# Kernel tuning notes

Hardware: AMD Instinct MI355X
Metric: run time of the kernel (lower is better)

The kernel has to match this reference:

```python
import jax, jax.numpy as jnp
import numpy as np

N = 524288          # total nodes (64 graphs x 8192 nodes)
E = 8388608         # total edges (avg degree 16)
F = 128             # num_features
H = 8               # hidden_size
B = 64              # num_graphs
NPG = N // B        # nodes per graph


def setup_inputs() -> dict:
    key = jax.random.key(0)
    ks = jax.random.split(key, 14)
    def lin(k, fan_in, shape):
        return (jax.random.normal(k, shape, jnp.float32) / np.float32(np.sqrt(fan_in)))
    return {
        "x": jax.random.normal(ks[0], (N, F), jnp.float32),
        "edge_index": jax.random.randint(ks[1], (2, E), 0, N, jnp.int32),
        "target_id": jax.random.randint(ks[2], (B,), 0, NPG, jnp.int32),
        "W1": lin(ks[3], F, (F, H)), "b1": jnp.zeros((H,), jnp.float32),
        "W2": lin(ks[4], H, (H, H)), "b2": jnp.zeros((H,), jnp.float32),
        "W3": lin(ks[5], H, (H, 1)), "b3": jnp.zeros((1,), jnp.float32),
        "Wl1": lin(ks[6], 2 * H + 1, (2 * H + 1, 16)), "bl1": jnp.zeros((16,), jnp.float32),
        "Wl2": lin(ks[7], 16, (16, 2)), "bl2": jnp.zeros((2,), jnp.float32),
    }


def reference(x, edge_index, target_id, W1, b1, W2, b2, W3, b3, Wl1, bl1, Wl2, bl2):
    src, dst = edge_index[0], edge_index[1]
    # GCN symmetric normalization with self-loops: deg includes the self-loop.
    deg = jax.ops.segment_sum(jnp.ones((E,), x.dtype), dst, num_segments=N) + 1.0
    dis = jax.lax.rsqrt(deg)                       # deg^{-1/2}, [N]
    norm = dis[src] * dis[dst]                     # per-edge coefficient, [E]

    def gcn_conv(h, W, b):
        h = h @ W                                  # [N, out]
        agg = jax.ops.segment_sum(h[src] * norm[:, None], dst, num_segments=N)
        # self-loop contribution has coefficient dis[i]*dis[i] = 1/deg[i]
        return agg + h * (dis * dis)[:, None] + b

    x1 = jax.nn.relu(gcn_conv(x, W1, b1))          # [N, 8]
    x2 = jax.nn.relu(gcn_conv(x1, W2, b2))         # [N, 8]
    x3 = jax.nn.relu(gcn_conv(x2, W3, b3))         # [N, 1]
    feats = jnp.concatenate([x1, x2, x3], axis=1)  # [N, 17]

    # per-graph target node: global index = graph_offset + local target_id
    idx = jnp.arange(B, dtype=jnp.int32) * NPG + target_id   # [B]
    z = jax.nn.relu(feats[idx] @ Wl1 + bl1)        # [B, 16]
    return z @ Wl2 + bl2                           # [B, 2]
```

## Files before the change

kernel.cpp:

```cpp
#include <hip/hip_runtime.h>
#include <cstdint>

#define N_NODES 524288
#define E_EDGES 8388608
#define F_IN 128
#define HID 8
#define B_GRAPHS 64
#define NPG 8192
#define NPG_SHIFT 13

#define BUCKETS 256
#define BSHIFT 11
#define BNODES 2048
#define BMASK 2047
#define SBLK 512
#define STHREADS 512
#define EPB (E_EDGES / SBLK)
#define CAP 160
#define EB_STRIDE (SBLK * CAP)
#define CSR_CAP 36864

__global__ void clear_kernel(int4* __restrict__ p) {
    p[blockIdx.x * blockDim.x + threadIdx.x] = make_int4(0, 0, 0, 0);
}

__global__ __launch_bounds__(STHREADS) void scatter_kernel(
        const int* __restrict__ src, const int* __restrict__ dst,
        unsigned int* __restrict__ ebuf, int* __restrict__ sc) {
    __shared__ int cur[BUCKETS];
    int t = threadIdx.x;
    if (t < BUCKETS) cur[t] = 0;
    __syncthreads();
    int eb = blockIdx.x * EPB;
    size_t blkoff = (size_t)blockIdx.x * CAP;
    #pragma unroll 4
    for (int k = 0; k < EPB / STHREADS; ++k) {
        int e = eb + k * STHREADS + t;
        int d = dst[e];
        int s = src[e];
        int b = d >> BSHIFT;
        int p = atomicAdd(&cur[b], 1);
        if (p < CAP)
            ebuf[(size_t)b * EB_STRIDE + blkoff + p] =
                ((unsigned int)(d & BMASK) << 19) | (unsigned int)s;
    }
    __syncthreads();
    if (t < BUCKETS) sc[t * SBLK + blockIdx.x] = (cur[t] < CAP) ? cur[t] : CAP;
}

__global__ __launch_bounds__(256) void build_kernel(const unsigned int* __restrict__ ebuf,
                                                    const int* __restrict__ sc,
                                                    int2* __restrict__ rowptr,
                                                    float* __restrict__ dis,
                                                    int* __restrict__ csr) {
    __shared__ int scs[SBLK];
    __shared__ int cnt[BNODES];
    __shared__ int cur[BNODES];
    __shared__ int tsum[256];
    int t = threadIdx.x;
    int b = blockIdx.x;
    for (int j = t; j < SBLK; j += 256) scs[j] = sc[b * SBLK + j];
    for (int j = t; j < BNODES; j += 256) cnt[j] = 0;
    __syncthreads();
    const unsigned int* eb = ebuf + (size_t)b * EB_STRIDE;
    int wv = t >> 6, ln = t & 63;
    for (int ss = wv; ss < SBLK; ss += 4) {
        int n = scs[ss];
        const unsigned int* p = eb + ss * CAP;
        for (int k = ln; k < n; k += 64)
            atomicAdd(&cnt[p[k] >> 19], 1);
    }
    __syncthreads();
    int v[8], loc[8], s = 0;
    #pragma unroll
    for (int k2 = 0; k2 < 8; ++k2) { v[k2] = cnt[t * 8 + k2]; loc[k2] = s; s += v[k2]; }
    tsum[t] = s;
    __syncthreads();
    for (int o = 1; o < 256; o <<= 1) {
        int y = (t >= o) ? tsum[t - o] : 0;
        __syncthreads();
        tsum[t] += y;
        __syncthreads();
    }
    int off = (t == 0) ? 0 : tsum[t - 1];
    int cbase = b * CSR_CAP;
    #pragma unroll
    for (int k2 = 0; k2 < 8; ++k2) {
        int j = t * 8 + k2;
        int st = off + loc[k2];
        cur[j] = st;
        rowptr[b * BNODES + j] = make_int2(cbase + st, cbase + st + v[k2]);
        dis[b * BNODES + j] = rsqrtf((float)v[k2] + 1.0f);
    }
    __syncthreads();
    for (int ss = wv; ss < SBLK; ss += 4) {
        int n = scs[ss];
        const unsigned int* p = eb + ss * CAP;
        for (int k = ln; k < n; k += 64) {
            unsigned int w = p[k];
            int ps = atomicAdd(&cur[w >> 19], 1);
            csr[cbase + ps] = (int)(w & 0x7FFFFu);
        }
    }
}

__global__ void bfs1_kernel(const int* __restrict__ tgt, const int2* __restrict__ rowptr,
                            const int* __restrict__ csr,
                            unsigned int* __restrict__ bm1, unsigned int* __restrict__ bm2,
                            unsigned int* __restrict__ bm3, unsigned int* __restrict__ bmT) {
    int g = threadIdx.x;
    if (g >= B_GRAPHS) return;
    int t = g * NPG + tgt[g];
    atomicOr(&bmT[t >> 5], 1u << (t & 31));
    atomicOr(&bm1[t >> 5], 1u << (t & 31));
    atomicOr(&bm2[t >> 5], 1u << (t & 31));
    atomicOr(&bm3[t >> 5], 1u << (t & 31));
    int2 r = rowptr[t];
    for (int k = r.x; k < r.y; ++k) {
        int s = csr[k];
        atomicOr(&bm1[s >> 5], 1u << (s & 31));
        atomicOr(&bm2[s >> 5], 1u << (s & 31));
        atomicOr(&bm3[s >> 5], 1u << (s & 31));
    }
}

__global__ void bfs2_kernel(const int2* __restrict__ rowptr, const int* __restrict__ csr,
                            const unsigned int* __restrict__ bm1,
                            unsigned int* __restrict__ bm2, unsigned int* __restrict__ bm3) {
    int i = blockIdx.x * blockDim.x + threadIdx.x;
    if (!((bm1[i >> 5] >> (i & 31)) & 1u)) return;
    int2 r = rowptr[i];
    for (int k = r.x; k < r.y; ++k) {
        int s = csr[k];
        atomicOr(&bm2[s >> 5], 1u << (s & 31));
        atomicOr(&bm3[s >> 5], 1u << (s & 31));
    }
}

__global__ void bfs3_kernel(const int2* __restrict__ rowptr, const int* __restrict__ csr,
                            const unsigned int* __restrict__ bm2,
                            unsigned int* __restrict__ bm3) {
    int i = blockIdx.x * blockDim.x + threadIdx.x;
    if (!((bm2[i >> 5] >> (i & 31)) & 1u)) return;
    int2 r = rowptr[i];
    for (int k = r.x; k < r.y; ++k) {
        int s = csr[k];
        atomicOr(&bm3[s >> 5], 1u << (s & 31));
    }
}

__global__ void mm1s_kernel(const float* __restrict__ x, const float* __restrict__ W1,
                            const unsigned int* __restrict__ bm3,
                            const float* __restrict__ dis, float* __restrict__ hps) {
    __shared__ float w[F_IN * HID];
    for (int t = threadIdx.x; t < F_IN * HID; t += blockDim.x) w[t] = W1[t];
    __syncthreads();
    int row = blockIdx.x * blockDim.x + threadIdx.x;
    if (!((bm3[row >> 5] >> (row & 31)) & 1u)) return;
    const float4* xr = (const float4*)(x + (size_t)row * F_IN);
    float acc[HID] = {0.f,0.f,0.f,0.f,0.f,0.f,0.f,0.f};
    #pragma unroll 8
    for (int it = 0; it < F_IN / 4; ++it) {
        float4 xv = xr[it];
        const float* wr = &w[it * 4 * HID];
        #pragma unroll
        for (int j = 0; j < HID; ++j)
            acc[j] += xv.x * wr[j] + xv.y * wr[HID + j] + xv.z * wr[2 * HID + j] + xv.w * wr[3 * HID + j];
    }
    float di = dis[row];
    float4* o = (float4*)(hps + (size_t)row * HID);
    o[0] = make_float4(acc[0] * di, acc[1] * di, acc[2] * di, acc[3] * di);
    o[1] = make_float4(acc[4] * di, acc[5] * di, acc[6] * di, acc[7] * di);
}

__global__ void gather1_kernel(const int2* __restrict__ rowptr, const int* __restrict__ csr,
                               const float* __restrict__ dis, const float* __restrict__ hps,
                               const unsigned int* __restrict__ bm2,
                               const unsigned int* __restrict__ bmT,
                               const float* __restrict__ b1v, const float* __restrict__ W2,
                               float* __restrict__ hps2, float* __restrict__ x1t) {
    __shared__ float w[HID * HID];
    if (threadIdx.x < HID * HID) w[threadIdx.x] = W2[threadIdx.x];
    __syncthreads();
    int i = blockIdx.x * blockDim.x + threadIdx.x;
    if (!((bm2[i >> 5] >> (i & 31)) & 1u)) return;
    float di = dis[i];
    int2 r = rowptr[i];
    float acc[HID] = {0.f,0.f,0.f,0.f,0.f,0.f,0.f,0.f};
    for (int k = r.x; k < r.y; ++k) {
        int s = csr[k];
        const float4* h = (const float4*)(hps + (size_t)s * HID);
        float4 a = h[0], b = h[1];
        acc[0] += a.x; acc[1] += a.y; acc[2] += a.z; acc[3] += a.w;
        acc[4] += b.x; acc[5] += b.y; acc[6] += b.z; acc[7] += b.w;
    }
    const float4* hs = (const float4*)(hps + (size_t)i * HID);
    float4 h0 = hs[0], h1 = hs[1];
    float v[HID];
    v[0] = fmaxf(di * (acc[0] + h0.x) + b1v[0], 0.f);
    v[1] = fmaxf(di * (acc[1] + h0.y) + b1v[1], 0.f);
    v[2] = fmaxf(di * (acc[2] + h0.z) + b1v[2], 0.f);
    v[3] = fmaxf(di * (acc[3] + h0.w) + b1v[3], 0.f);
    v[4] = fmaxf(di * (acc[4] + h1.x) + b1v[4], 0.f);
    v[5] = fmaxf(di * (acc[5] + h1.y) + b1v[5], 0.f);
    v[6] = fmaxf(di * (acc[6] + h1.z) + b1v[6], 0.f);
    v[7] = fmaxf(di * (acc[7] + h1.w) + b1v[7], 0.f);
    if ((bmT[i >> 5] >> (i & 31)) & 1u) {
        float* xt = x1t + (size_t)(i >> NPG_SHIFT) * HID;
        #pragma unroll
        for (int j = 0; j < HID; ++j) xt[j] = v[j];
    }
    float o[HID];
    #pragma unroll
    for (int j = 0; j < HID; ++j) {
        float sj = 0.f;
        #pragma unroll
        for (int k = 0; k < HID; ++k) sj += v[k] * w[k * HID + j];
        o[j] = sj * di;
    }
    float4* op = (float4*)(hps2 + (size_t)i * HID);
    op[0] = make_float4(o[0], o[1], o[2], o[3]);
    op[1] = make_float4(o[4], o[5], o[6], o[7]);
}

__global__ void gather2_kernel(const int2* __restrict__ rowptr, const int* __restrict__ csr,
                               const float* __restrict__ dis, const float* __restrict__ hps2,
                               const unsigned int* __restrict__ bm1,
                               const float* __restrict__ b2v, float* __restrict__ x2) {
    int i = blockIdx.x * blockDim.x + threadIdx.x;
    if (!((bm1[i >> 5] >> (i & 31)) & 1u)) return;
    float di = dis[i];
    int2 r = rowptr[i];
    float acc[HID] = {0.f,0.f,0.f,0.f,0.f,0.f,0.f,0.f};
    for (int k = r.x; k < r.y; ++k) {
        int s = csr[k];
        const float4* h = (const float4*)(hps2 + (size_t)s * HID);
        float4 a = h[0], b = h[1];
        acc[0] += a.x; acc[1] += a.y; acc[2] += a.z; acc[3] += a.w;
        acc[4] += b.x; acc[5] += b.y; acc[6] += b.z; acc[7] += b.w;
    }
    const float4* hs = (const float4*)(hps2 + (size_t)i * HID);
    float4 h0 = hs[0], h1 = hs[1];
    float4* xo = (float4*)(x2 + (size_t)i * HID);
    xo[0] = make_float4(fmaxf(di * (acc[0] + h0.x) + b2v[0], 0.f),
                        fmaxf(di * (acc[1] + h0.y) + b2v[1], 0.f),
                        fmaxf(di * (acc[2] + h0.z) + b2v[2], 0.f),
                        fmaxf(di * (acc[3] + h0.w) + b2v[3], 0.f));
    xo[1] = make_float4(fmaxf(di * (acc[4] + h1.x) + b2v[4], 0.f),
                        fmaxf(di * (acc[5] + h1.y) + b2v[5], 0.f),
                        fmaxf(di * (acc[6] + h1.z) + b2v[6], 0.f),
                        fmaxf(di * (acc[7] + h1.w) + b2v[7], 0.f));
}

__global__ void headf_kernel(const int* __restrict__ tgt, const int2* __restrict__ rowptr,
                             const int* __restrict__ csr, const float* __restrict__ dis,
                             const float* __restrict__ x1t, const float* __restrict__ x2,
                             const float* __restrict__ W3, const float* __restrict__ b3,
                             const float* __restrict__ Wl1, const float* __restrict__ bl1,
                             const float* __restrict__ Wl2, const float* __restrict__ bl2,
                             float* __restrict__ out) {
    int g = threadIdx.x;
    if (g >= B_GRAPHS) return;
    size_t t = (size_t)g * NPG + tgt[g];
    float di = dis[t];
    float w3[HID];
    #pragma unroll
    for (int j = 0; j < HID; ++j) w3[j] = W3[j];
    float f[17];
    #pragma unroll
    for (int j = 0; j < HID; ++j) f[j] = x1t[(size_t)g * HID + j];
    #pragma unroll
    for (int j = 0; j < HID; ++j) f[8 + j] = x2[t * HID + j];
    int2 r = rowptr[t];
    float a3 = 0.f;
    for (int k = r.x; k < r.y; ++k) {
        int s = csr[k];
        float h = 0.f;
        #pragma unroll
        for (int j = 0; j < HID; ++j) h += x2[(size_t)s * HID + j] * w3[j];
        a3 += h * dis[s];
    }
    float h3 = 0.f;
    #pragma unroll
    for (int j = 0; j < HID; ++j) h3 += f[8 + j] * w3[j];
    f[16] = fmaxf(a3 * di + h3 * di * di + b3[0], 0.f);
    float o0 = bl2[0], o1 = bl2[1];
    #pragma unroll
    for (int j = 0; j < 16; ++j) {
        float z = bl1[j];
        #pragma unroll
        for (int k = 0; k < 17; ++k) z += f[k] * Wl1[k * 16 + j];
        z = fmaxf(z, 0.f);
        o0 += z * Wl2[j * 2 + 0];
        o1 += z * Wl2[j * 2 + 1];
    }
    out[g * 2 + 0] = o0;
    out[g * 2 + 1] = o1;
}

extern "C" void kernel_launch(void* const* d_in, const int* in_sizes, int n_in,
                              void* d_out, int out_size, void* d_ws, size_t ws_size,
                              hipStream_t stream) {
    const float* x  = (const float*)d_in[0];
    const int* ei   = (const int*)d_in[1];
    const int* src  = ei;
    const int* dst  = ei + E_EDGES;
    const int* tid  = (const int*)d_in[2];
    const float* W1 = (const float*)d_in[3];
    const float* b1 = (const float*)d_in[4];
    const float* W2 = (const float*)d_in[5];
    const float* b2 = (const float*)d_in[6];
    const float* W3 = (const float*)d_in[7];
    const float* b3 = (const float*)d_in[8];
    const float* Wl1 = (const float*)d_in[9];
    const float* bl1 = (const float*)d_in[10];
    const float* Wl2 = (const float*)d_in[11];
    const float* bl2 = (const float*)d_in[12];
    float* out = (float*)d_out;

    char* ws = (char*)d_ws;
    size_t off = 0;
    auto alloc = [&](size_t bytes) {
        void* p = ws + off;
        off += (bytes + 255) & ~(size_t)255;
        return p;
    };
    unsigned int* bm1 = (unsigned int*)alloc(65536);
    unsigned int* bm2 = (unsigned int*)alloc(65536);
    unsigned int* bm3 = (unsigned int*)alloc(65536);
    unsigned int* bmT = (unsigned int*)alloc(65536);
    float* x1t  = (float*)alloc((size_t)B_GRAPHS * HID * 4);
    int* sc     = (int*)alloc((size_t)BUCKETS * SBLK * 4);
    int2* rowptr = (int2*)alloc((size_t)N_NODES * 8);
    float* dis  = (float*)alloc((size_t)N_NODES * 4);
    unsigned int* ebuf = (unsigned int*)alloc((size_t)BUCKETS * EB_STRIDE * 4);
    int* csr    = (int*)alloc((size_t)BUCKETS * CSR_CAP * 4);
    float* hps  = (float*)alloc((size_t)N_NODES * HID * 4);
    float* hps2 = (float*)alloc((size_t)N_NODES * HID * 4);
    float* x2 = hps;
    (void)ws_size;

    clear_kernel<<<64, 256, 0, stream>>>((int4*)bm1);
    scatter_kernel<<<SBLK, STHREADS, 0, stream>>>(src, dst, ebuf, sc);
    build_kernel<<<BUCKETS, 256, 0, stream>>>(ebuf, sc, rowptr, dis, csr);
    bfs1_kernel<<<1, 64, 0, stream>>>(tid, rowptr, csr, bm1, bm2, bm3, bmT);
    bfs2_kernel<<<2048, 256, 0, stream>>>(rowptr, csr, bm1, bm2, bm3);
    bfs3_kernel<<<2048, 256, 0, stream>>>(rowptr, csr, bm2, bm3);
    mm1s_kernel<<<2048, 256, 0, stream>>>(x, W1, bm3, dis, hps);
    gather1_kernel<<<2048, 256, 0, stream>>>(rowptr, csr, dis, hps, bm2, bmT, b1, W2, hps2, x1t);
    gather2_kernel<<<2048, 256, 0, stream>>>(rowptr, csr, dis, hps2, bm1, b2, x2);
    headf_kernel<<<1, 64, 0, stream>>>(tid, rowptr, csr, dis, x1t, x2,
                                       W3, b3, Wl1, bl1, Wl2, bl2, out);
}
```

Baseline: 783.7 us.

## Replace full CSR build and BFS with edge-list sweeps building only needed CSR rows

```diff
diff --git a/kernel.cpp b/kernel.cpp
--- a/kernel.cpp
+++ b/kernel.cpp
@@ -18,14 +18,27 @@
 #define EPB (E_EDGES / SBLK)
 #define CAP 160
 #define EB_STRIDE (SBLK * CAP)
-#define CSR_CAP 36864
+
+#define SWBLK 8192
 
 __global__ void clear_kernel(int4* __restrict__ p) {
     p[blockIdx.x * blockDim.x + threadIdx.x] = make_int4(0, 0, 0, 0);
 }
 
+__global__ void init_kernel(const int* __restrict__ tgt,
+                            unsigned int* __restrict__ bmT, unsigned int* __restrict__ bmP1,
+                            unsigned int* __restrict__ bmP2, unsigned int* __restrict__ bmP3) {
+    int g = threadIdx.x;
+    if (g >= B_GRAPHS) return;
+    int t = g * NPG + tgt[g];
+    atomicOr(&bmT[t >> 5], 1u << (t & 31));
+    atomicOr(&bmP1[t >> 5], 1u << (t & 31));
+    atomicOr(&bmP2[t >> 5], 1u << (t & 31));
+    atomicOr(&bmP3[t >> 5], 1u << (t & 31));
+}
+
 __global__ __launch_bounds__(STHREADS) void scatter_kernel(
-        const int* __restrict__ src, const int* __restrict__ dst,
+        const int* __restrict__ dst,
         unsigned int* __restrict__ ebuf, int* __restrict__ sc) {
     __shared__ int cur[BUCKETS];
     int t = threadIdx.x;
@@ -35,27 +48,23 @@
     size_t blkoff = (size_t)blockIdx.x * CAP;
     #pragma unroll 4
     for (int k = 0; k < EPB / STHREADS; ++k) {
-        int e = eb + k * STHREADS + t;
-        int d = dst[e];
-        int s = src[e];
+        int d = dst[eb + k * STHREADS + t];
         int b = d >> BSHIFT;
         int p = atomicAdd(&cur[b], 1);
         if (p < CAP)
-            ebuf[(size_t)b * EB_STRIDE + blkoff + p] =
-                ((unsigned int)(d & BMASK) << 19) | (unsigned int)s;
+            ebuf[(size_t)b * EB_STRIDE + blkoff + p] = (unsigned int)(d & BMASK);
     }
     __syncthreads();
     if (t < BUCKETS) sc[t * SBLK + blockIdx.x] = (cur[t] < CAP) ? cur[t] : CAP;
 }
 
-__global__ __launch_bounds__(256) void build_kernel(const unsigned int* __restrict__ ebuf,
+__global__ __launch_bounds__(256) void count_kernel(const unsigned int* __restrict__ ebuf,
                                                     const int* __restrict__ sc,
-                                                    int2* __restrict__ rowptr,
+                                                    int2* __restrict__ rowptr2,
                                                     float* __restrict__ dis,
-                                                    int* __restrict__ csr) {
+                                                    int* __restrict__ btot) {
     __shared__ int scs[SBLK];
     __shared__ int cnt[BNODES];
-    __shared__ int cur[BNODES];
     __shared__ int tsum[256];
     int t = threadIdx.x;
     int b = blockIdx.x;
@@ -68,7 +77,7 @@
         int n = scs[ss];
         const unsigned int* p = eb + ss * CAP;
         for (int k = ln; k < n; k += 64)
-            atomicAdd(&cnt[p[k] >> 19], 1);
+            atomicAdd(&cnt[p[k]], 1);
     }
     __syncthreads();
     int v[8], loc[8], s = 0;
@@ -83,80 +92,99 @@
         __syncthreads();
     }
     int off = (t == 0) ? 0 : tsum[t - 1];
-    int cbase = b * CSR_CAP;
     #pragma unroll
     for (int k2 = 0; k2 < 8; ++k2) {
         int j = t * 8 + k2;
         int st = off + loc[k2];
-        cur[j] = st;
-        rowptr[b * BNODES + j] = make_int2(cbase + st, cbase + st + v[k2]);
+        rowptr2[b * BNODES + j] = make_int2(st, st + v[k2]);
         dis[b * BNODES + j] = rsqrtf((float)v[k2] + 1.0f);
     }
-    __syncthreads();
-    for (int ss = wv; ss < SBLK; ss += 4) {
-        int n = scs[ss];
-        const unsigned int* p = eb + ss * CAP;
-        for (int k = ln; k < n; k += 64) {
-            unsigned int w = p[k];
-            int ps = atomicAdd(&cur[w >> 19], 1);
-            csr[cbase + ps] = (int)(w & 0x7FFFFu);
+    if (t == 255) btot[b] = off + s;
+}
+
+__global__ void basescan_kernel(const int* __restrict__ btot, int* __restrict__ bbase) {
+    __shared__ int tsum[256];
+    int t = threadIdx.x;
+    int v = btot[t];
+    tsum[t] = v;
+    __syncthreads();
+    for (int o = 1; o < 256; o <<= 1) {
+        int y = (t >= o) ? tsum[t - o] : 0;
+        __syncthreads();
+        tsum[t] += y;
+        __syncthreads();
+    }
+    int off = tsum[t] - v;
+    bbase[t] = off;
+    if (t == 255) bbase[256] = off + v;
+}
+
+__global__ __launch_bounds__(256) void sweep1_kernel(
+        const int* __restrict__ src, const int* __restrict__ dst,
+        const unsigned int* __restrict__ bmT,
+        unsigned int* __restrict__ bmP1, unsigned int* __restrict__ bmP2,
+        unsigned int* __restrict__ bmP3) {
+    int i = blockIdx.x * 256 + threadIdx.x;
+    int4 d4 = ((const int4*)dst)[i];
+    int e = i * 4;
+    #pragma unroll
+    for (int k = 0; k < 4; ++k) {
+        int d = (k == 0) ? d4.x : (k == 1) ? d4.y : (k == 2) ? d4.z : d4.w;
+        if ((bmT[d >> 5] >> (d & 31)) & 1u) {
+            int s = src[e + k];
+            atomicOr(&bmP1[s >> 5], 1u << (s & 31));
+            atomicOr(&bmP2[s >> 5], 1u << (s & 31));
+            atomicOr(&bmP3[s >> 5], 1u << (s & 31));
         }
     }
 }
 
-__global__ void bfs1_kernel(const int* __restrict__ tgt, const int2* __restrict__ rowptr,
-                            const int* __restrict__ csr,
-                            unsigned int* __restrict__ bm1, unsigned int* __restrict__ bm2,
-                            unsigned int* __restrict__ bm3, unsigned int* __restrict__ bmT) {
-    int g = threadIdx.x;
-    if (g >= B_GRAPHS) return;
-    int t = g * NPG + tgt[g];
-    atomicOr(&bmT[t >> 5], 1u << (t & 31));
-    atomicOr(&bm1[t >> 5], 1u << (t & 31));
-    atomicOr(&bm2[t >> 5], 1u << (t & 31));
-    atomicOr(&bm3[t >> 5], 1u << (t & 31));
-    int2 r = rowptr[t];
-    for (int k = r.x; k < r.y; ++k) {
-        int s = csr[k];
-        atomicOr(&bm1[s >> 5], 1u << (s & 31));
-        atomicOr(&bm2[s >> 5], 1u << (s & 31));
-        atomicOr(&bm3[s >> 5], 1u << (s & 31));
-    }
-}
-
-__global__ void bfs2_kernel(const int2* __restrict__ rowptr, const int* __restrict__ csr,
-                            const unsigned int* __restrict__ bm1,
-                            unsigned int* __restrict__ bm2, unsigned int* __restrict__ bm3) {
-    int i = blockIdx.x * blockDim.x + threadIdx.x;
-    if (!((bm1[i >> 5] >> (i & 31)) & 1u)) return;
-    int2 r = rowptr[i];
-    for (int k = r.x; k < r.y; ++k) {
-        int s = csr[k];
-        atomicOr(&bm2[s >> 5], 1u << (s & 31));
-        atomicOr(&bm3[s >> 5], 1u << (s & 31));
-    }
-}
-
-__global__ void bfs3_kernel(const int2* __restrict__ rowptr, const int* __restrict__ csr,
-                            const unsigned int* __restrict__ bm2,
-                            unsigned int* __restrict__ bm3) {
-    int i = blockIdx.x * blockDim.x + threadIdx.x;
-    if (!((bm2[i >> 5] >> (i & 31)) & 1u)) return;
-    int2 r = rowptr[i];
-    for (int k = r.x; k < r.y; ++k) {
-        int s = csr[k];
-        atomicOr(&bm3[s >> 5], 1u << (s & 31));
+__global__ __launch_bounds__(256) void sweep2_kernel(
+        const int* __restrict__ src, const int* __restrict__ dst,
+        const unsigned int* __restrict__ bmP1,
+        unsigned int* __restrict__ bmP2, unsigned int* __restrict__ bmP3) {
+    int i = blockIdx.x * 256 + threadIdx.x;
+    int4 d4 = ((const int4*)dst)[i];
+    int e = i * 4;
+    #pragma unroll
+    for (int k = 0; k < 4; ++k) {
+        int d = (k == 0) ? d4.x : (k == 1) ? d4.y : (k == 2) ? d4.z : d4.w;
+        if ((bmP1[d >> 5] >> (d & 31)) & 1u) {
+            int s = src[e + k];
+            atomicOr(&bmP2[s >> 5], 1u << (s & 31));
+            atomicOr(&bmP3[s >> 5], 1u << (s & 31));
+        }
+    }
+}
+
+__global__ __launch_bounds__(256) void sweep3_kernel(
+        const int* __restrict__ src, const int* __restrict__ dst,
+        const unsigned int* __restrict__ bmP2, unsigned int* __restrict__ bmP3,
+        const int2* __restrict__ rowptr2, const int* __restrict__ bbase,
+        int* __restrict__ cur, int* __restrict__ csr) {
+    int i = blockIdx.x * 256 + threadIdx.x;
+    int4 d4 = ((const int4*)dst)[i];
+    int e = i * 4;
+    #pragma unroll
+    for (int k = 0; k < 4; ++k) {
+        int d = (k == 0) ? d4.x : (k == 1) ? d4.y : (k == 2) ? d4.z : d4.w;
+        if ((bmP2[d >> 5] >> (d & 31)) & 1u) {
+            int s = src[e + k];
+            atomicOr(&bmP3[s >> 5], 1u << (s & 31));
+            int p = atomicAdd(&cur[d], 1);
+            csr[bbase[d >> BSHIFT] + rowptr2[d].x + p] = s;
+        }
     }
 }
 
 __global__ void mm1s_kernel(const float* __restrict__ x, const float* __restrict__ W1,
-                            const unsigned int* __restrict__ bm3,
+                            const unsigned int* __restrict__ bmP3,
                             const float* __restrict__ dis, float* __restrict__ hps) {
     __shared__ float w[F_IN * HID];
     for (int t = threadIdx.x; t < F_IN * HID; t += blockDim.x) w[t] = W1[t];
     __syncthreads();
     int row = blockIdx.x * blockDim.x + threadIdx.x;
-    if (!((bm3[row >> 5] >> (row & 31)) & 1u)) return;
+    if (!((bmP3[row >> 5] >> (row & 31)) & 1u)) return;
     const float4* xr = (const float4*)(x + (size_t)row * F_IN);
     float acc[HID] = {0.f,0.f,0.f,0.f,0.f,0.f,0.f,0.f};
     #pragma unroll 8
@@ -173,9 +201,10 @@
     o[1] = make_float4(acc[4] * di, acc[5] * di, acc[6] * di, acc[7] * di);
 }
 
-__global__ void gather1_kernel(const int2* __restrict__ rowptr, const int* __restrict__ csr,
+__global__ void gather1_kernel(const int2* __restrict__ rowptr2, const int* __restrict__ bbase,
+                               const int* __restrict__ csr,
                                const float* __restrict__ dis, const float* __restrict__ hps,
-                               const unsigned int* __restrict__ bm2,
+                               const unsigned int* __restrict__ bmP2,
                                const unsigned int* __restrict__ bmT,
                                const float* __restrict__ b1v, const float* __restrict__ W2,
                                float* __restrict__ hps2, float* __restrict__ x1t) {
@@ -183,11 +212,13 @@
     if (threadIdx.x < HID * HID) w[threadIdx.x] = W2[threadIdx.x];
     __syncthreads();
     int i = blockIdx.x * blockDim.x + threadIdx.x;
-    if (!((bm2[i >> 5] >> (i & 31)) & 1u)) return;
+    if (!((bmP2[i >> 5] >> (i & 31)) & 1u)) return;
     float di = dis[i];
-    int2 r = rowptr[i];
+    int2 r = rowptr2[i];
+    int bb = bbase[i >> BSHIFT];
+    int e0 = bb + r.x, e1 = bb + r.y;
     float acc[HID] = {0.f,0.f,0.f,0.f,0.f,0.f,0.f,0.f};
-    for (int k = r.x; k < r.y; ++k) {
+    for (int k = e0; k < e1; ++k) {
         int s = csr[k];
         const float4* h = (const float4*)(hps + (size_t)s * HID);
         float4 a = h[0], b = h[1];
@@ -223,16 +254,19 @@
     op[1] = make_float4(o[4], o[5], o[6], o[7]);
 }
 
-__global__ void gather2_kernel(const int2* __restrict__ rowptr, const int* __restrict__ csr,
+__global__ void gather2_kernel(const int2* __restrict__ rowptr2, const int* __restrict__ bbase,
+                               const int* __restrict__ csr,
                                const float* __restrict__ dis, const float* __restrict__ hps2,
-                               const unsigned int* __restrict__ bm1,
+                               const unsigned int* __restrict__ bmP1,
                                const float* __restrict__ b2v, float* __restrict__ x2) {
     int i = blockIdx.x * blockDim.x + threadIdx.x;
-    if (!((bm1[i >> 5] >> (i & 31)) & 1u)) return;
+    if (!((bmP1[i >> 5] >> (i & 31)) & 1u)) return;
     float di = dis[i];
-    int2 r = rowptr[i];
+    int2 r = rowptr2[i];
+    int bb = bbase[i >> BSHIFT];
+    int e0 = bb + r.x, e1 = bb + r.y;
     float acc[HID] = {0.f,0.f,0.f,0.f,0.f,0.f,0.f,0.f};
-    for (int k = r.x; k < r.y; ++k) {
+    for (int k = e0; k < e1; ++k) {
         int s = csr[k];
         const float4* h = (const float4*)(hps2 + (size_t)s * HID);
         float4 a = h[0], b = h[1];
@@ -252,8 +286,9 @@
                         fmaxf(di * (acc[7] + h1.w) + b2v[7], 0.f));
 }
 
-__global__ void headf_kernel(const int* __restrict__ tgt, const int2* __restrict__ rowptr,
-                             const int* __restrict__ csr, const float* __restrict__ dis,
+__global__ void headf_kernel(const int* __restrict__ tgt, const int2* __restrict__ rowptr2,
+                             const int* __restrict__ bbase, const int* __restrict__ csr,
+                             const float* __restrict__ dis,
                              const float* __restrict__ x1t, const float* __restrict__ x2,
                              const float* __restrict__ W3, const float* __restrict__ b3,
                              const float* __restrict__ Wl1, const float* __restrict__ bl1,
@@ -271,9 +306,10 @@
     for (int j = 0; j < HID; ++j) f[j] = x1t[(size_t)g * HID + j];
     #pragma unroll
     for (int j = 0; j < HID; ++j) f[8 + j] = x2[t * HID + j];
-    int2 r = rowptr[t];
+    int2 r = rowptr2[t];
+    int bb = bbase[t >> BSHIFT];
     float a3 = 0.f;
-    for (int k = r.x; k < r.y; ++k) {
+    for (int k = bb + r.x; k < bb + r.y; ++k) {
         int s = csr[k];
         float h = 0.f;
         #pragma unroll
@@ -325,30 +361,36 @@
         off += (bytes + 255) & ~(size_t)255;
         return p;
     };
-    unsigned int* bm1 = (unsigned int*)alloc(65536);
-    unsigned int* bm2 = (unsigned int*)alloc(65536);
-    unsigned int* bm3 = (unsigned int*)alloc(65536);
-    unsigned int* bmT = (unsigned int*)alloc(65536);
-    float* x1t  = (float*)alloc((size_t)B_GRAPHS * HID * 4);
-    int* sc     = (int*)alloc((size_t)BUCKETS * SBLK * 4);
-    int2* rowptr = (int2*)alloc((size_t)N_NODES * 8);
-    float* dis  = (float*)alloc((size_t)N_NODES * 4);
+    unsigned int* bmT  = (unsigned int*)alloc(65536);
+    unsigned int* bmP1 = (unsigned int*)alloc(65536);
+    unsigned int* bmP2 = (unsigned int*)alloc(65536);
+    unsigned int* bmP3 = (unsigned int*)alloc(65536);
+    int* cur = (int*)alloc((size_t)N_NODES * 4);
+    const int CLEAR_INT4 = (4 * 65536 + N_NODES * 4) / 16;
+    float* x1t   = (float*)alloc((size_t)B_GRAPHS * HID * 4);
+    int* sc      = (int*)alloc((size_t)BUCKETS * SBLK * 4);
+    int* btot    = (int*)alloc((size_t)BUCKETS * 4);
+    int* bbase   = (int*)alloc((size_t)(BUCKETS + 1) * 4);
+    int2* rowptr2 = (int2*)alloc((size_t)N_NODES * 8);
+    float* dis   = (float*)alloc((size_t)N_NODES * 4);
     unsigned int* ebuf = (unsigned int*)alloc((size_t)BUCKETS * EB_STRIDE * 4);
-    int* csr    = (int*)alloc((size_t)BUCKETS * CSR_CAP * 4);
-    float* hps  = (float*)alloc((size_t)N_NODES * HID * 4);
-    float* hps2 = (float*)alloc((size_t)N_NODES * HID * 4);
+    int* csr     = (int*)alloc((size_t)E_EDGES * 4);
+    float* hps   = (float*)alloc((size_t)N_NODES * HID * 4);
+    float* hps2  = (float*)alloc((size_t)N_NODES * HID * 4);
     float* x2 = hps;
     (void)ws_size;
 
-    clear_kernel<<<64, 256, 0, stream>>>((int4*)bm1);
-    scatter_kernel<<<SBLK, STHREADS, 0, stream>>>(src, dst, ebuf, sc);
-    build_kernel<<<BUCKETS, 256, 0, stream>>>(ebuf, sc, rowptr, dis, csr);
-    bfs1_kernel<<<1, 64, 0, stream>>>(tid, rowptr, csr, bm1, bm2, bm3, bmT);
-    bfs2_kernel<<<2048, 256, 0, stream>>>(rowptr, csr, bm1, bm2, bm3);
-    bfs3_kernel<<<2048, 256, 0, stream>>>(rowptr, csr, bm2, bm3);
-    mm1s_kernel<<<2048, 256, 0, stream>>>(x, W1, bm3, dis, hps);
-    gather1_kernel<<<2048, 256, 0, stream>>>(rowptr, csr, dis, hps, bm2, bmT, b1, W2, hps2, x1t);
-    gather2_kernel<<<2048, 256, 0, stream>>>(rowptr, csr, dis, hps2, bm1, b2, x2);
-    headf_kernel<<<1, 64, 0, stream>>>(tid, rowptr, csr, dis, x1t, x2,
+    clear_kernel<<<CLEAR_INT4 / 256, 256, 0, stream>>>((int4*)bmT);
+    init_kernel<<<1, 64, 0, stream>>>(tid, bmT, bmP1, bmP2, bmP3);
+    scatter_kernel<<<SBLK, STHREADS, 0, stream>>>(dst, ebuf, sc);
+    count_kernel<<<BUCKETS, 256, 0, stream>>>(ebuf, sc, rowptr2, dis, btot);
+    basescan_kernel<<<1, 256, 0, stream>>>(btot, bbase);
+    sweep1_kernel<<<SWBLK, 256, 0, stream>>>(src, dst, bmT, bmP1, bmP2, bmP3);
+    sweep2_kernel<<<SWBLK, 256, 0, stream>>>(src, dst, bmP1, bmP2, bmP3);
+    sweep3_kernel<<<SWBLK, 256, 0, stream>>>(src, dst, bmP2, bmP3, rowptr2, bbase, cur, csr);
+    mm1s_kernel<<<2048, 256, 0, stream>>>(x, W1, bmP3, dis, hps);
+    gather1_kernel<<<2048, 256, 0, stream>>>(rowptr2, bbase, csr, dis, hps, bmP2, bmT, b1, W2, hps2, x1t);
+    gather2_kernel<<<2048, 256, 0, stream>>>(rowptr2, bbase, csr, dis, hps2, bmP1, b2, x2);
+    headf_kernel<<<1, 64, 0, stream>>>(tid, rowptr2, bbase, csr, dis, x1t, x2,
                                        W3, b3, Wl1, bl1, Wl2, bl2, out);
 }
```

Measured after the change: 752.7 us. 3.9% less time.

## Stage bucket edges in shared memory and use finer buckets for CSR build

Applied to the files above, without the earlier changes.

```diff
diff --git a/kernel.cpp b/kernel.cpp
--- a/kernel.cpp
+++ b/kernel.cpp
@@ -9,16 +9,17 @@
 #define NPG 8192
 #define NPG_SHIFT 13
 
-#define BUCKETS 256
-#define BSHIFT 11
-#define BNODES 2048
-#define BMASK 2047
-#define SBLK 512
+#define BUCKETS 512
+#define BSHIFT 10
+#define BNODES 1024
+#define LMASK 1023
+#define SBLK 1024
 #define STHREADS 512
 #define EPB (E_EDGES / SBLK)
-#define CAP 160
+#define CAP 64
 #define EB_STRIDE (SBLK * CAP)
-#define CSR_CAP 36864
+#define SBUF_CAP 18432
+#define CSR_CAP 18432
 
 __global__ void clear_kernel(int4* __restrict__ p) {
     p[blockIdx.x * blockDim.x + threadIdx.x] = make_int4(0, 0, 0, 0);
@@ -29,7 +30,7 @@
         unsigned int* __restrict__ ebuf, int* __restrict__ sc) {
     __shared__ int cur[BUCKETS];
     int t = threadIdx.x;
-    if (t < BUCKETS) cur[t] = 0;
+    cur[t] = 0;
     __syncthreads();
     int eb = blockIdx.x * EPB;
     size_t blkoff = (size_t)blockIdx.x * CAP;
@@ -42,10 +43,10 @@
         int p = atomicAdd(&cur[b], 1);
         if (p < CAP)
             ebuf[(size_t)b * EB_STRIDE + blkoff + p] =
-                ((unsigned int)(d & BMASK) << 19) | (unsigned int)s;
-    }
-    __syncthreads();
-    if (t < BUCKETS) sc[t * SBLK + blockIdx.x] = (cur[t] < CAP) ? cur[t] : CAP;
+                ((unsigned int)(d & LMASK) << 19) | (unsigned int)s;
+    }
+    __syncthreads();
+    sc[t * SBLK + blockIdx.x] = (cur[t] < CAP) ? cur[t] : CAP;
 }
 
 __global__ __launch_bounds__(256) void build_kernel(const unsigned int* __restrict__ ebuf,
@@ -53,28 +54,19 @@
                                                     int2* __restrict__ rowptr,
                                                     float* __restrict__ dis,
                                                     int* __restrict__ csr) {
-    __shared__ int scs[SBLK];
+    __shared__ int soff[SBLK];
+    __shared__ unsigned int sbuf[SBUF_CAP];
     __shared__ int cnt[BNODES];
     __shared__ int cur[BNODES];
     __shared__ int tsum[256];
+    __shared__ int ntot_s;
     int t = threadIdx.x;
     int b = blockIdx.x;
-    for (int j = t; j < SBLK; j += 256) scs[j] = sc[b * SBLK + j];
-    for (int j = t; j < BNODES; j += 256) cnt[j] = 0;
-    __syncthreads();
-    const unsigned int* eb = ebuf + (size_t)b * EB_STRIDE;
-    int wv = t >> 6, ln = t & 63;
-    for (int ss = wv; ss < SBLK; ss += 4) {
-        int n = scs[ss];
-        const unsigned int* p = eb + ss * CAP;
-        for (int k = ln; k < n; k += 64)
-            atomicAdd(&cnt[p[k] >> 19], 1);
-    }
-    __syncthreads();
-    int v[8], loc[8], s = 0;
-    #pragma unroll
-    for (int k2 = 0; k2 < 8; ++k2) { v[k2] = cnt[t * 8 + k2]; loc[k2] = s; s += v[k2]; }
+    int4 c4 = ((const int4*)(sc + (size_t)b * SBLK))[t];
+    int n0 = c4.x, n1 = c4.y, n2 = c4.z, n3 = c4.w;
+    int s = n0 + n1 + n2 + n3;
     tsum[t] = s;
+    cnt[t * 4 + 0] = 0; cnt[t * 4 + 1] = 0; cnt[t * 4 + 2] = 0; cnt[t * 4 + 3] = 0;
     __syncthreads();
     for (int o = 1; o < 256; o <<= 1) {
         int y = (t >= o) ? tsum[t - o] : 0;
@@ -83,24 +75,55 @@
         __syncthreads();
     }
     int off = (t == 0) ? 0 : tsum[t - 1];
+    soff[t * 4 + 0] = off;
+    soff[t * 4 + 1] = off + n0;
+    soff[t * 4 + 2] = off + n0 + n1;
+    soff[t * 4 + 3] = off + n0 + n1 + n2;
+    if (t == 255) ntot_s = tsum[255];
+    __syncthreads();
+    const unsigned int* eb = ebuf + (size_t)b * EB_STRIDE;
+    #pragma unroll
+    for (int k2 = 0; k2 < 4; ++k2) {
+        int ss = t * 4 + k2;
+        int n = (k2 == 0) ? n0 : (k2 == 1) ? n1 : (k2 == 2) ? n2 : n3;
+        int so = soff[ss];
+        if (so + n > SBUF_CAP) n = (SBUF_CAP > so) ? (SBUF_CAP - so) : 0;
+        const unsigned int* p = eb + (size_t)ss * CAP;
+        for (int k = 0; k < n; ++k) {
+            unsigned int w = p[k];
+            sbuf[so + k] = w;
+            atomicAdd(&cnt[w >> 19], 1);
+        }
+    }
+    __syncthreads();
+    int v[4], loc[4], s2 = 0;
+    #pragma unroll
+    for (int k2 = 0; k2 < 4; ++k2) { v[k2] = cnt[t * 4 + k2]; loc[k2] = s2; s2 += v[k2]; }
+    tsum[t] = s2;
+    __syncthreads();
+    for (int o = 1; o < 256; o <<= 1) {
+        int y = (t >= o) ? tsum[t - o] : 0;
+        __syncthreads();
+        tsum[t] += y;
+        __syncthreads();
+    }
+    int off2 = (t == 0) ? 0 : tsum[t - 1];
     int cbase = b * CSR_CAP;
     #pragma unroll
-    for (int k2 = 0; k2 < 8; ++k2) {
-        int j = t * 8 + k2;
-        int st = off + loc[k2];
+    for (int k2 = 0; k2 < 4; ++k2) {
+        int j = t * 4 + k2;
+        int st = off2 + loc[k2];
         cur[j] = st;
         rowptr[b * BNODES + j] = make_int2(cbase + st, cbase + st + v[k2]);
         dis[b * BNODES + j] = rsqrtf((float)v[k2] + 1.0f);
     }
     __syncthreads();
-    for (int ss = wv; ss < SBLK; ss += 4) {
-        int n = scs[ss];
-        const unsigned int* p = eb + ss * CAP;
-        for (int k = ln; k < n; k += 64) {
-            unsigned int w = p[k];
-            int ps = atomicAdd(&cur[w >> 19], 1);
-            csr[cbase + ps] = (int)(w & 0x7FFFFu);
-        }
+    int ntot = ntot_s;
+    if (ntot > SBUF_CAP) ntot = SBUF_CAP;
+    for (int k = t; k < ntot; k += 256) {
+        unsigned int w = sbuf[k];
+        int p = atomicAdd(&cur[w >> 19], 1);
+        csr[cbase + p] = (int)(w & 0x7FFFFu);
     }
 }
 
@@ -325,30 +348,30 @@
         off += (bytes + 255) & ~(size_t)255;
         return p;
     };
-    unsigned int* bm1 = (unsigned int*)alloc(65536);
-    unsigned int* bm2 = (unsigned int*)alloc(65536);
-    unsigned int* bm3 = (unsigned int*)alloc(65536);
-    unsigned int* bmT = (unsigned int*)alloc(65536);
-    float* x1t  = (float*)alloc((size_t)B_GRAPHS * HID * 4);
-    int* sc     = (int*)alloc((size_t)BUCKETS * SBLK * 4);
+    unsigned int* bmT  = (unsigned int*)alloc(65536);
+    unsigned int* bmP1 = (unsigned int*)alloc(65536);
+    unsigned int* bmP2 = (unsigned int*)alloc(65536);
+    unsigned int* bmP3 = (unsigned int*)alloc(65536);
+    float* x1t   = (float*)alloc((size_t)B_GRAPHS * HID * 4);
+    int* sc      = (int*)alloc((size_t)BUCKETS * SBLK * 4);
     int2* rowptr = (int2*)alloc((size_t)N_NODES * 8);
-    float* dis  = (float*)alloc((size_t)N_NODES * 4);
+    float* dis   = (float*)alloc((size_t)N_NODES * 4);
     unsigned int* ebuf = (unsigned int*)alloc((size_t)BUCKETS * EB_STRIDE * 4);
-    int* csr    = (int*)alloc((size_t)BUCKETS * CSR_CAP * 4);
-    float* hps  = (float*)alloc((size_t)N_NODES * HID * 4);
-    float* hps2 = (float*)alloc((size_t)N_NODES * HID * 4);
+    int* csr     = (int*)alloc((size_t)BUCKETS * CSR_CAP * 4);
+    float* hps   = (float*)alloc((size_t)N_NODES * HID * 4);
+    float* hps2  = (float*)alloc((size_t)N_NODES * HID * 4);
     float* x2 = hps;
     (void)ws_size;
 
-    clear_kernel<<<64, 256, 0, stream>>>((int4*)bm1);
+    clear_kernel<<<64, 256, 0, stream>>>((int4*)bmT);
     scatter_kernel<<<SBLK, STHREADS, 0, stream>>>(src, dst, ebuf, sc);
     build_kernel<<<BUCKETS, 256, 0, stream>>>(ebuf, sc, rowptr, dis, csr);
-    bfs1_kernel<<<1, 64, 0, stream>>>(tid, rowptr, csr, bm1, bm2, bm3, bmT);
-    bfs2_kernel<<<2048, 256, 0, stream>>>(rowptr, csr, bm1, bm2, bm3);
-    bfs3_kernel<<<2048, 256, 0, stream>>>(rowptr, csr, bm2, bm3);
-    mm1s_kernel<<<2048, 256, 0, stream>>>(x, W1, bm3, dis, hps);
-    gather1_kernel<<<2048, 256, 0, stream>>>(rowptr, csr, dis, hps, bm2, bmT, b1, W2, hps2, x1t);
-    gather2_kernel<<<2048, 256, 0, stream>>>(rowptr, csr, dis, hps2, bm1, b2, x2);
+    bfs1_kernel<<<1, 64, 0, stream>>>(tid, rowptr, csr, bmP1, bmP2, bmP3, bmT);
+    bfs2_kernel<<<2048, 256, 0, stream>>>(rowptr, csr, bmP1, bmP2, bmP3);
+    bfs3_kernel<<<2048, 256, 0, stream>>>(rowptr, csr, bmP2, bmP3);
+    mm1s_kernel<<<2048, 256, 0, stream>>>(x, W1, bmP3, dis, hps);
+    gather1_kernel<<<2048, 256, 0, stream>>>(rowptr, csr, dis, hps, bmP2, bmT, b1, W2, hps2, x1t);
+    gather2_kernel<<<2048, 256, 0, stream>>>(rowptr, csr, dis, hps2, bmP1, b2, x2);
     headf_kernel<<<1, 64, 0, stream>>>(tid, rowptr, csr, dis, x1t, x2,
                                        W3, b3, Wl1, bl1, Wl2, bl2, out);
 }
```

Result: faster. 729.8 us (-6.9%).
